# Performance work log

Hardware: AMD Instinct MI355X
Metric: run time of the kernel (lower is better)

The kernel has to match this reference:

```python
import jax, jax.numpy as jnp
import numpy as np

D_MODEL = 1024
N_HEADS = 16


def setup_inputs() -> dict:
    key = jax.random.key(0)
    ks = jax.random.split(key, 11)
    B, S, D = 2, 2048, D_MODEL
    scale = 1.0 / np.sqrt(D)
    inp = {
        "q": jax.random.normal(ks[0], (B, S, D), jnp.float32),
        "k": jax.random.normal(ks[1], (B, S, D), jnp.float32),
        "v": jax.random.normal(ks[2], (B, S, D), jnp.float32),
        "W_q": jax.random.normal(ks[3], (D, D), jnp.float32) * scale,
        "b_q": jnp.zeros((D,), jnp.float32),
        "W_k": jax.random.normal(ks[4], (D, D), jnp.float32) * scale,
        "b_k": jnp.zeros((D,), jnp.float32),
        "W_v": jax.random.normal(ks[5], (D, D), jnp.float32) * scale,
        "b_v": jnp.zeros((D,), jnp.float32),
        "W_o": jax.random.normal(ks[6], (D, D), jnp.float32) * scale,
        "b_o": jnp.zeros((D,), jnp.float32),
    }
    return inp


def reference(q, k, v, W_q, b_q, W_k, b_k, W_v, b_v, W_o, b_o):
    B, S, D = q.shape
    H = N_HEADS
    d_k = D // H
    # linear projections, then split heads: [B, H, S, d_k]
    def proj(x, W, b):
        y = jnp.einsum("bsd,de->bse", x, W.T) + b
        return y.reshape(B, S, H, d_k).transpose(0, 2, 1, 3)
    Q = proj(q, W_q, b_q)
    K = proj(k, W_k, b_k)
    V = proj(v, W_v, b_v)
    # scaled dot-product attention with explicit [B,H,S,S] scores
    scores = jnp.einsum("bhqd,bhkd->bhqk", Q, K) / jnp.sqrt(jnp.float32(d_k))
    attn = jax.nn.softmax(scores, axis=-1)
    out = jnp.einsum("bhqk,bhkd->bhqd", attn, V)
    out = out.transpose(0, 2, 1, 3).reshape(B, S, D)
    return jnp.einsum("bsd,de->bse", out, W_o.T) + b_o
```

## Files before the change

### kernel.cpp

```cpp
#include <hip/hip_runtime.h>
#include <hip/hip_bf16.h>
#include <math.h>

typedef __bf16 bf16_t;
typedef bf16_t bf16x8 __attribute__((ext_vector_type(8)));
typedef float f32x4 __attribute__((ext_vector_type(4)));

#define D_MODEL 1024
#define NH 16
#define DK 64
#define SEQ 2048
#define MROWS 4096
#define LDSW 64
#define LDC 136

__device__ __forceinline__ bf16x8 ldfrag(const bf16_t* p) {
    union { uint4 u; bf16x8 v; } c;
    c.u = *reinterpret_cast<const uint4*>(p);
    return c.v;
}

__device__ __forceinline__ f32x4 zero4() { f32x4 z = {0.f, 0.f, 0.f, 0.f}; return z; }

__device__ __forceinline__ void gll16(const bf16_t* g, bf16_t* l) {
    __builtin_amdgcn_global_load_lds(
        (const __attribute__((address_space(1))) unsigned int*)g,
        (__attribute__((address_space(3))) unsigned int*)l,
        16, 0, 0);
}

__global__ void pack3(const float* __restrict__ a, const float* __restrict__ b,
                      const float* __restrict__ c,
                      bf16_t* __restrict__ da, bf16_t* __restrict__ db, bf16_t* __restrict__ dc) {
    const float* s = (blockIdx.y == 0) ? a : (blockIdx.y == 1) ? b : c;
    bf16_t* d      = (blockIdx.y == 0) ? da : (blockIdx.y == 1) ? db : dc;
    int i = (blockIdx.x * blockDim.x + threadIdx.x) * 4;
    float4 f = *reinterpret_cast<const float4*>(s + i);
    union { bf16_t h[4]; uint2 u; } o;
    o.h[0] = (bf16_t)f.x; o.h[1] = (bf16_t)f.y; o.h[2] = (bf16_t)f.z; o.h[3] = (bf16_t)f.w;
    *reinterpret_cast<uint2*>(d + i) = o.u;
}

__global__ void pack4(const float* __restrict__ a, const float* __restrict__ b,
                      const float* __restrict__ c, const float* __restrict__ e,
                      bf16_t* __restrict__ da, bf16_t* __restrict__ db,
                      bf16_t* __restrict__ dc, bf16_t* __restrict__ de) {
    const float* s = (blockIdx.y == 0) ? a : (blockIdx.y == 1) ? b : (blockIdx.y == 2) ? c : e;
    bf16_t* d      = (blockIdx.y == 0) ? da : (blockIdx.y == 1) ? db : (blockIdx.y == 2) ? dc : de;
    int i = (blockIdx.x * blockDim.x + threadIdx.x) * 4;
    float4 f = *reinterpret_cast<const float4*>(s + i);
    union { bf16_t h[4]; uint2 u; } o;
    o.h[0] = (bf16_t)f.x; o.h[1] = (bf16_t)f.y; o.h[2] = (bf16_t)f.z; o.h[3] = (bf16_t)f.w;
    *reinterpret_cast<uint2*>(d + i) = o.u;
}

__device__ __forceinline__ void gemm_core(
    const bf16_t* __restrict__ A, const bf16_t* __restrict__ Bm,
    int K, int m0, int n0,
    bf16_t* As, bf16_t* Bs,
    f32x4 acc[4][4]) {

    const int tid = threadIdx.x;
    const int lane = tid & 63;
    const int wid = tid >> 6;
    const int wm = (wid >> 1) * 64, wn = (wid & 1) * 64;
    const int l15 = lane & 15, quad = lane >> 4;

    const int lrow   = lane >> 3;
    const int gcol   = ((lane & 7) ^ lrow) * 8;

    #pragma unroll
    for (int i = 0; i < 4; i++)
        #pragma unroll
        for (int j = 0; j < 4; j++) acc[i][j] = zero4();

    for (int k0 = 0; k0 < K; k0 += 64) {
        __syncthreads();
        #pragma unroll
        for (int t = 0; t < 4; t++) {
            const int rbase = wid * 32 + t * 8;
            gll16(A  + (size_t)(m0 + rbase + lrow) * K + k0 + gcol, As + rbase * LDSW);
            gll16(Bm + (size_t)(n0 + rbase + lrow) * K + k0 + gcol, Bs + rbase * LDSW);
        }
        __syncthreads();
        #pragma unroll
        for (int c = 0; c < 2; c++) {
            bf16x8 af[4], bfr[4];
            #pragma unroll
            for (int i = 0; i < 4; i++) {
                const int row = wm + i * 16 + l15;
                const int pc = ((c * 4 + quad) ^ (l15 & 7)) * 8;
                af[i] = ldfrag(As + row * LDSW + pc);
            }
            #pragma unroll
            for (int j = 0; j < 4; j++) {
                const int row = wn + j * 16 + l15;
                const int pc = ((c * 4 + quad) ^ (l15 & 7)) * 8;
                bfr[j] = ldfrag(Bs + row * LDSW + pc);
            }
            #pragma unroll
            for (int i = 0; i < 4; i++)
                #pragma unroll
                for (int j = 0; j < 4; j++)
                    acc[i][j] = __builtin_amdgcn_mfma_f32_16x16x32_bf16(af[i], bfr[j], acc[i][j], 0, 0, 0);
        }
    }
}

__global__ __launch_bounds__(256, 2) void proj_gemm(
    const bf16_t* __restrict__ qb, const bf16_t* __restrict__ kb,
    const bf16_t* __restrict__ vb,
    const bf16_t* __restrict__ Wq, const bf16_t* __restrict__ Wk,
    const bf16_t* __restrict__ Wv,
    const float* __restrict__ bq, const float* __restrict__ bk, const float* __restrict__ bv,
    bf16_t* __restrict__ Qh, bf16_t* __restrict__ Kh, bf16_t* __restrict__ Vt) {

    __shared__ __align__(16) bf16_t sm[128 * LDC];
    bf16_t* As = sm;
    bf16_t* Bs = sm + 128 * LDSW;
    bf16_t (*Cs)[LDC] = reinterpret_cast<bf16_t(*)[LDC]>(sm);
    f32x4 acc[4][4];

    const int mode = blockIdx.z;
    const bf16_t* X = (mode == 0) ? qb : (mode == 1) ? kb : vb;
    const bf16_t* W = (mode == 0) ? Wq : (mode == 1) ? Wk : Wv;
    const float* bias = (mode == 0) ? bq : (mode == 1) ? bk : bv;
    const int m0 = blockIdx.y * 128, n0 = blockIdx.x * 128;

    gemm_core(X, W, D_MODEL, m0, n0, As, Bs, acc);

    const int tid = threadIdx.x, lane = tid & 63, wid = tid >> 6;
    const int wm = (wid >> 1) * 64, wn = (wid & 1) * 64;
    const int l15 = lane & 15, quad = lane >> 4;

    __syncthreads();
    if (mode != 2) {
        const float sc = (mode == 0) ? 0.125f * 1.44269504f : 1.0f;
        #pragma unroll
        for (int i = 0; i < 4; i++)
            #pragma unroll
            for (int j = 0; j < 4; j++)
                #pragma unroll
                for (int r = 0; r < 4; r++) {
                    int gn = n0 + wn + j * 16 + l15;
                    Cs[wm + i * 16 + quad * 4 + r][wn + j * 16 + l15] =
                        (bf16_t)((acc[i][j][r] + bias[gn]) * sc);
                }
    } else {
        #pragma unroll
        for (int i = 0; i < 4; i++)
            #pragma unroll
            for (int j = 0; j < 4; j++)
                #pragma unroll
                for (int r = 0; r < 4; r++) {
                    int gn = n0 + wn + j * 16 + l15;
                    Cs[wn + j * 16 + l15][wm + i * 16 + quad * 4 + r] =
                        (bf16_t)(acc[i][j][r] + bias[gn]);
                }
    }
    __syncthreads();

    #pragma unroll
    for (int c = tid; c < 2048; c += 256) {
        int row = c >> 4, col8 = (c & 15) << 3;
        uint4 val = *reinterpret_cast<const uint4*>(&Cs[row][col8]);
        if (mode != 2) {
            int gm = m0 + row, gn = n0 + col8;
            int b = gm >> 11, seq = gm & 2047;
            int h = gn >> 6, dk = gn & 63;
            bf16_t* dst = (mode == 0) ? Qh : Kh;
            *reinterpret_cast<uint4*>(dst + ((size_t)(b * NH + h) * SEQ + seq) * DK + dk) = val;
        } else {
            int gn = n0 + row, gm = m0 + col8;
            int b = gm >> 11, seq = gm & 2047;
            int h = gn >> 6, dk = gn & 63;
            *reinterpret_cast<uint4*>(Vt + ((size_t)(b * NH + h) * DK + dk) * SEQ + seq) = val;
        }
    }
}

__global__ __launch_bounds__(256, 2) void out_gemm(
    const bf16_t* __restrict__ Oc, const bf16_t* __restrict__ Wo,
    const float* __restrict__ bo, float* __restrict__ Cout) {

    __shared__ __align__(16) bf16_t As[128 * LDSW];
    __shared__ __align__(16) bf16_t Bs[128 * LDSW];
    f32x4 acc[4][4];
    const int m0 = blockIdx.y * 128, n0 = blockIdx.x * 128;

    gemm_core(Oc, Wo, D_MODEL, m0, n0, As, Bs, acc);

    const int tid = threadIdx.x, lane = tid & 63, wid = tid >> 6;
    const int wm = (wid >> 1) * 64, wn = (wid & 1) * 64;
    const int l15 = lane & 15, quad = lane >> 4;

    #pragma unroll
    for (int i = 0; i < 4; i++)
        #pragma unroll
        for (int j = 0; j < 4; j++)
            #pragma unroll
            for (int r = 0; r < 4; r++) {
                int gm = m0 + wm + i * 16 + quad * 4 + r;
                int gn = n0 + wn + j * 16 + l15;
                Cout[(size_t)gm * D_MODEL + gn] = acc[i][j][r] + bo[gn];
            }
}

__global__ __launch_bounds__(256) void attn_kernel(
    const bf16_t* __restrict__ Qh, const bf16_t* __restrict__ Kh,
    const bf16_t* __restrict__ Vt, bf16_t* __restrict__ Oc) {

    __shared__ __align__(16) bf16_t Ks[2][64 * LDSW];
    __shared__ __align__(16) bf16_t Vts[2][64 * LDSW];
    __shared__ __align__(16) bf16_t Pls[64 * LDSW];

    const int tid = threadIdx.x, lane = tid & 63, wid = tid >> 6;
    const int l15 = lane & 15, quad = lane >> 4;
    const int bh = blockIdx.x;
    const int q0 = blockIdx.y * 64;
    const bf16_t* Qbase = Qh + (size_t)bh * SEQ * DK;
    const bf16_t* Kbase = Kh + (size_t)bh * SEQ * DK;
    const bf16_t* Vbase = Vt + (size_t)bh * DK * SEQ;

    const int lrow = lane >> 3;
    const int gcol = ((lane & 7) ^ lrow) * 8;

    bf16x8 aQ[2];
    #pragma unroll
    for (int c = 0; c < 2; c++)
        aQ[c] = ldfrag(Qbase + (size_t)(q0 + wid * 16 + l15) * DK + c * 32 + quad * 8);

    f32x4 oacc[4];
    #pragma unroll
    for (int j = 0; j < 4; j++) oacc[j] = zero4();
    float l_i[4] = {0.f, 0.f, 0.f, 0.f};

    #pragma unroll
    for (int t = 0; t < 2; t++) {
        const int rbase = wid * 16 + t * 8;
        gll16(Kbase + (size_t)(rbase + lrow) * DK + gcol,  Ks[0]  + rbase * LDSW);
        gll16(Vbase + (size_t)(rbase + lrow) * SEQ + gcol, Vts[0] + rbase * LDSW);
    }

    const int pch = l15 >> 3, pwi = l15 & 7;

    for (int kt = 0; kt < SEQ / 64; kt++) {
        const int buf = kt & 1;
        const int nkt = (kt + 1 < SEQ / 64) ? kt + 1 : kt;
        const int nk0 = nkt * 64;

        #pragma unroll
        for (int t = 0; t < 2; t++) {
            const int rbase = wid * 16 + t * 8;
            gll16(Kbase + (size_t)(nk0 + rbase + lrow) * DK + gcol,  Ks[buf ^ 1]  + rbase * LDSW);
            gll16(Vbase + (size_t)(rbase + lrow) * SEQ + nk0 + gcol, Vts[buf ^ 1] + rbase * LDSW);
        }
        asm volatile("s_waitcnt vmcnt(4)" ::: "memory");
        __builtin_amdgcn_s_barrier();
        __builtin_amdgcn_sched_barrier(0);

        const bf16_t* Kb = Ks[buf];
        const bf16_t* Vb = Vts[buf];

        f32x4 sacc[4];
        #pragma unroll
        for (int j = 0; j < 4; j++) sacc[j] = zero4();
        __builtin_amdgcn_s_setprio(1);
        #pragma unroll
        for (int c = 0; c < 2; c++) {
            bf16x8 bk4[4];
            #pragma unroll
            for (int j = 0; j < 4; j++) {
                const int pc = ((c * 4 + quad) ^ (l15 & 7)) * 8;
                bk4[j] = ldfrag(Kb + (j * 16 + l15) * LDSW + pc);
            }
            #pragma unroll
            for (int j = 0; j < 4; j++)
                sacc[j] = __builtin_amdgcn_mfma_f32_16x16x32_bf16(
                    aQ[c], bk4[j], sacc[j], 0, 0, 0);
        }
        __builtin_amdgcn_s_setprio(0);

        #pragma unroll
        for (int r = 0; r < 4; r++) {
            float e0 = exp2f(sacc[0][r]);
            float e1 = exp2f(sacc[1][r]);
            float e2 = exp2f(sacc[2][r]);
            float e3 = exp2f(sacc[3][r]);
            l_i[r] += (e0 + e1) + (e2 + e3);
            bf16_t* prow = Pls + (wid * 16 + quad * 4 + r) * LDSW;
            const int rx = (quad * 4 + r) & 7;
            prow[((pch    ) ^ rx) * 8 + pwi] = (bf16_t)e0;
            prow[((pch + 2) ^ rx) * 8 + pwi] = (bf16_t)e1;
            prow[((pch + 4) ^ rx) * 8 + pwi] = (bf16_t)e2;
            prow[((pch + 6) ^ rx) * 8 + pwi] = (bf16_t)e3;
        }

        __builtin_amdgcn_s_setprio(1);
        #pragma unroll
        for (int c = 0; c < 2; c++) {
            bf16x8 ap = ldfrag(Pls + (wid * 16 + l15) * LDSW +
                               (((c * 4 + quad) ^ (l15 & 7)) << 3));
            bf16x8 bv4[4];
            #pragma unroll
            for (int j = 0; j < 4; j++) {
                const int pc = ((c * 4 + quad) ^ (l15 & 7)) * 8;
                bv4[j] = ldfrag(Vb + (j * 16 + l15) * LDSW + pc);
            }
            #pragma unroll
            for (int j = 0; j < 4; j++)
                oacc[j] = __builtin_amdgcn_mfma_f32_16x16x32_bf16(
                    ap, bv4[j], oacc[j], 0, 0, 0);
        }
        __builtin_amdgcn_s_setprio(0);

        __builtin_amdgcn_s_barrier();
    }

    #pragma unroll
    for (int r = 0; r < 4; r++) {
        float l = l_i[r];
        #pragma unroll
        for (int off = 1; off < 16; off <<= 1)
            l += __shfl_xor(l, off, 64);
        float inv = 1.0f / l;
        bf16_t* prow = Pls + (wid * 16 + quad * 4 + r) * LDSW;
        const int rx = (quad * 4 + r) & 7;
        #pragma unroll
        for (int j = 0; j < 4; j++)
            prow[((pch + 2 * j) ^ rx) * 8 + pwi] = (bf16_t)(oacc[j][r] * inv);
    }
    __syncthreads();

    const int b = bh >> 4, h = bh & 15;
    #pragma unroll
    for (int c = tid; c < 512; c += 256) {
        int row = c >> 3, chunk = c & 7;
        uint4 val = *reinterpret_cast<const uint4*>(
            Pls + row * LDSW + ((chunk ^ (row & 7)) << 3));
        *reinterpret_cast<uint4*>(Oc + ((size_t)(b * SEQ + q0 + row)) * D_MODEL + h * DK + (chunk << 3)) = val;
    }
}

extern "C" void kernel_launch(void* const* d_in, const int* in_sizes, int n_in,
                              void* d_out, int out_size, void* d_ws, size_t ws_size,
                              hipStream_t stream) {
    const float* q  = (const float*)d_in[0];
    const float* k  = (const float*)d_in[1];
    const float* v  = (const float*)d_in[2];
    const float* Wq = (const float*)d_in[3];
    const float* bq = (const float*)d_in[4];
    const float* Wk = (const float*)d_in[5];
    const float* bk = (const float*)d_in[6];
    const float* Wv = (const float*)d_in[7];
    const float* bv = (const float*)d_in[8];
    const float* Wo = (const float*)d_in[9];
    const float* bo = (const float*)d_in[10];

    const size_t nx = (size_t)MROWS * D_MODEL;
    const size_t nw = (size_t)D_MODEL * D_MODEL;

    bf16_t* qb  = (bf16_t*)d_ws;
    bf16_t* kb  = qb  + nx;
    bf16_t* vb  = kb  + nx;
    bf16_t* Wqb = vb  + nx;
    bf16_t* Wkb = Wqb + nw;
    bf16_t* Wvb = Wkb + nw;
    bf16_t* Wob = Wvb + nw;
    bf16_t* Qh  = Wob + nw;
    bf16_t* Kh  = Qh  + nx;
    bf16_t* Vt  = Kh  + nx;
    bf16_t* Oc  = Vt  + nx;

    pack3<<<dim3(4096, 3), 256, 0, stream>>>(q, k, v, qb, kb, vb);
    pack4<<<dim3(1024, 4), 256, 0, stream>>>(Wq, Wk, Wv, Wo, Wqb, Wkb, Wvb, Wob);

    proj_gemm<<<dim3(8, 32, 3), 256, 0, stream>>>(qb, kb, vb, Wqb, Wkb, Wvb, bq, bk, bv, Qh, Kh, Vt);
    attn_kernel<<<dim3(32, 32), 256, 0, stream>>>(Qh, Kh, Vt, Oc);
    out_gemm<<<dim3(8, 32), 256, 0, stream>>>(Oc, Wob, bo, (float*)d_out);
}
```

Measured before the change: 261.5 us.

## Single-buffer K/V tiles in attention with staggered per-phase prefetch

Replaces the double-buffered K and V shared-memory tiles with single buffers. The next K tile is loaded right after QK^T finishes, and the next V tile right after PV finishes, each behind a full wait and barrier. This halves K/V LDS usage, which could allow more resident blocks per CU. In exchange it adds a second barrier per iteration and full vmcnt(0) waits that expose load latency. It also drops the s_setprio hints.

```diff
diff --git a/kernel.cpp b/kernel.cpp
--- a/kernel.cpp
+++ b/kernel.cpp
@@ -210,8 +210,8 @@
     const bf16_t* __restrict__ Qh, const bf16_t* __restrict__ Kh,
     const bf16_t* __restrict__ Vt, bf16_t* __restrict__ Oc) {
 
-    __shared__ __align__(16) bf16_t Ks[2][64 * LDSW];
-    __shared__ __align__(16) bf16_t Vts[2][64 * LDSW];
+    __shared__ __align__(16) bf16_t Ks[64 * LDSW];
+    __shared__ __align__(16) bf16_t Vts[64 * LDSW];
     __shared__ __align__(16) bf16_t Pls[64 * LDSW];
 
     const int tid = threadIdx.x, lane = tid & 63, wid = tid >> 6;
@@ -238,48 +238,44 @@
     #pragma unroll
     for (int t = 0; t < 2; t++) {
         const int rbase = wid * 16 + t * 8;
-        gll16(Kbase + (size_t)(rbase + lrow) * DK + gcol,  Ks[0]  + rbase * LDSW);
-        gll16(Vbase + (size_t)(rbase + lrow) * SEQ + gcol, Vts[0] + rbase * LDSW);
-    }
+        gll16(Kbase + (size_t)(rbase + lrow) * DK + gcol,  Ks  + rbase * LDSW);
+        gll16(Vbase + (size_t)(rbase + lrow) * SEQ + gcol, Vts + rbase * LDSW);
+    }
+    __syncthreads();
 
     const int pch = l15 >> 3, pwi = l15 & 7;
-
-    for (int kt = 0; kt < SEQ / 64; kt++) {
-        const int buf = kt & 1;
-        const int nkt = (kt + 1 < SEQ / 64) ? kt + 1 : kt;
-        const int nk0 = nkt * 64;
-
-        #pragma unroll
-        for (int t = 0; t < 2; t++) {
-            const int rbase = wid * 16 + t * 8;
-            gll16(Kbase + (size_t)(nk0 + rbase + lrow) * DK + gcol,  Ks[buf ^ 1]  + rbase * LDSW);
-            gll16(Vbase + (size_t)(rbase + lrow) * SEQ + nk0 + gcol, Vts[buf ^ 1] + rbase * LDSW);
-        }
-        asm volatile("s_waitcnt vmcnt(4)" ::: "memory");
-        __builtin_amdgcn_s_barrier();
-        __builtin_amdgcn_sched_barrier(0);
-
-        const bf16_t* Kb = Ks[buf];
-        const bf16_t* Vb = Vts[buf];
-
+    const int NT = SEQ / 64;
+
+    for (int kt = 0; kt < NT; kt++) {
         f32x4 sacc[4];
         #pragma unroll
         for (int j = 0; j < 4; j++) sacc[j] = zero4();
-        __builtin_amdgcn_s_setprio(1);
         #pragma unroll
         for (int c = 0; c < 2; c++) {
             bf16x8 bk4[4];
             #pragma unroll
             for (int j = 0; j < 4; j++) {
                 const int pc = ((c * 4 + quad) ^ (l15 & 7)) * 8;
-                bk4[j] = ldfrag(Kb + (j * 16 + l15) * LDSW + pc);
+                bk4[j] = ldfrag(Ks + (j * 16 + l15) * LDSW + pc);
             }
             #pragma unroll
             for (int j = 0; j < 4; j++)
                 sacc[j] = __builtin_amdgcn_mfma_f32_16x16x32_bf16(
                     aQ[c], bk4[j], sacc[j], 0, 0, 0);
         }
-        __builtin_amdgcn_s_setprio(0);
+
+        asm volatile("s_waitcnt vmcnt(0) lgkmcnt(0)" ::: "memory");
+        __builtin_amdgcn_s_barrier();
+        __builtin_amdgcn_sched_barrier(0);
+
+        if (kt + 1 < NT) {
+            const int nk0 = (kt + 1) * 64;
+            #pragma unroll
+            for (int t = 0; t < 2; t++) {
+                const int rbase = wid * 16 + t * 8;
+                gll16(Kbase + (size_t)(nk0 + rbase + lrow) * DK + gcol, Ks + rbase * LDSW);
+            }
+        }
 
         #pragma unroll
         for (int r = 0; r < 4; r++) {
@@ -296,7 +292,6 @@
             prow[((pch + 6) ^ rx) * 8 + pwi] = (bf16_t)e3;
         }
 
-        __builtin_amdgcn_s_setprio(1);
         #pragma unroll
         for (int c = 0; c < 2; c++) {
             bf16x8 ap = ldfrag(Pls + (wid * 16 + l15) * LDSW +
@@ -305,16 +300,26 @@
             #pragma unroll
             for (int j = 0; j < 4; j++) {
                 const int pc = ((c * 4 + quad) ^ (l15 & 7)) * 8;
-                bv4[j] = ldfrag(Vb + (j * 16 + l15) * LDSW + pc);
+                bv4[j] = ldfrag(Vts + (j * 16 + l15) * LDSW + pc);
             }
             #pragma unroll
             for (int j = 0; j < 4; j++)
                 oacc[j] = __builtin_amdgcn_mfma_f32_16x16x32_bf16(
                     ap, bv4[j], oacc[j], 0, 0, 0);
         }
-        __builtin_amdgcn_s_setprio(0);
-
+
+        asm volatile("s_waitcnt vmcnt(0) lgkmcnt(0)" ::: "memory");
         __builtin_amdgcn_s_barrier();
+        __builtin_amdgcn_sched_barrier(0);
+
+        if (kt + 1 < NT) {
+            const int nk0 = (kt + 1) * 64;
+            #pragma unroll
+            for (int t = 0; t < 2; t++) {
+                const int rbase = wid * 16 + t * 8;
+                gll16(Vbase + (size_t)(rbase + lrow) * SEQ + nk0 + gcol, Vts + rbase * LDSW);
+            }
+        }
     }
 
     #pragma unroll
```

Result: no change. 258.3 us (-1.2%).
